# Kernel tuning notes

Measured on AMD Instinct MI355X. Metric: run time of the kernel, lower is better.

## Reference

```python
import jax, jax.numpy as jnp
import numpy as np

B, F, K, DEPTH = 512, 64, 64, 3  # feas == k == 64, deepDepth == 3


def setup_inputs() -> dict:
    key = jax.random.key(0)
    ks = jax.random.split(key, 16)
    x = jax.random.normal(ks[0], (B, F), dtype=jnp.float32)
    # wide: Linear(feas, 1)
    Ww = jax.random.normal(ks[1], (1, F), dtype=jnp.float32) * 0.1
    bw = jnp.zeros((1,), dtype=jnp.float32)
    # cross: Parameter(torch.rand(feas, k))
    cross = jax.random.uniform(ks[2], (F, K), dtype=jnp.float32)
    # attention: Linear(k, k) -> ReLU -> Linear(k, 1, bias=False)
    W1 = jax.random.normal(ks[3], (K, K), dtype=jnp.float32) / np.sqrt(K)
    b1 = jnp.zeros((K,), dtype=jnp.float32)
    w2 = jax.random.normal(ks[4], (K,), dtype=jnp.float32) / np.sqrt(K)
    # deep{i}: Linear(k//i, k//(i+1)) + ReLU, i = 1..DEPTH  -> 64->32->21->16
    dims = [K // i for i in range(1, DEPTH + 2)]  # [64, 32, 21, 16]
    Wd1 = jax.random.normal(ks[5], (dims[1], dims[0]), dtype=jnp.float32) / np.sqrt(dims[0])
    bd1 = jnp.zeros((dims[1],), dtype=jnp.float32)
    Wd2 = jax.random.normal(ks[6], (dims[2], dims[1]), dtype=jnp.float32) / np.sqrt(dims[1])
    bd2 = jnp.zeros((dims[2],), dtype=jnp.float32)
    Wd3 = jax.random.normal(ks[7], (dims[3], dims[2]), dtype=jnp.float32) / np.sqrt(dims[2])
    bd3 = jnp.zeros((dims[3],), dtype=jnp.float32)
    # out: Linear(feas // (deepDepth+1), 1) == Linear(16, 1)
    Wo = jax.random.normal(ks[8], (1, F // (DEPTH + 1)), dtype=jnp.float32) * 0.1
    bo = jnp.zeros((1,), dtype=jnp.float32)
    return {"x": x, "Ww": Ww, "bw": bw, "cross": cross, "W1": W1, "b1": b1,
            "w2": w2, "Wd1": Wd1, "bd1": bd1, "Wd2": Wd2, "bd2": bd2,
            "Wd3": Wd3, "bd3": bd3, "Wo": Wo, "bo": bo}


def reference(x, Ww, bw, cross, W1, b1, w2, Wd1, bd1, Wd2, bd2, Wd3, bd3, Wo, bo):
    linear = x @ Ww.T + bw  # [B, 1]

    # Pairwise FM interactions v[b,i,j,:] = x_i * x_j * (cross_i ∘ cross_j)
    xx = x[:, :, None] * x[:, None, :]                    # [B, F, F]
    cp = cross[:, None, :] * cross[None, :, :]            # [F, F, K]
    v = xx[..., None] * cp[None]                          # [B, F, F, K]

    # attention MLP score per pair
    h = jax.nn.relu(jnp.einsum('bijk,lk->bijl', v, W1) + b1)
    s = jnp.einsum('bijl,l->bij', h, w2)                  # [B, F, F]

    # loop semantics: upper triangle (j >= i), pair kept iff x_i != 0 and x_j != 0
    valid = jnp.triu(jnp.ones((F, F), dtype=bool))[None] \
        & (x[:, :, None] != 0) & (x[:, None, :] != 0)     # [B, F, F]
    neg = jnp.finfo(s.dtype).min
    logits = jnp.where(valid, s, neg)

    # softmax over [0 (seed zeros(1) entry), valid pair scores...];
    # the seed zeros(k) value-vector contributes nothing to the weighted sum.
    m = jnp.maximum(jnp.max(logits, axis=(1, 2)), 0.0)    # [B]
    e = jnp.where(valid, jnp.exp(logits - m[:, None, None]), 0.0)
    denom = jnp.exp(-m) + jnp.sum(e, axis=(1, 2))         # +exp(-m) is the 0-logit term
    tmp = jnp.einsum('bij,bijk->bk', e, v) / denom[:, None]  # [B, K]

    tmp = jax.nn.relu(tmp @ Wd1.T + bd1)
    tmp = jax.nn.relu(tmp @ Wd2.T + bd2)
    tmp = jax.nn.relu(tmp @ Wd3.T + bd3)
    deep_out = tmp @ Wo.T + bo                            # [B, 1]
    return jax.nn.sigmoid(linear + deep_out)
```

## Files before the change

kernel.cpp:

```cpp
#include <hip/hip_runtime.h>
#include <math.h>


#define BB 512
#define FF 64
#define STR 68
#define NPAIRS 2080
#define THREADS 512
#define NIT2 65
#define NEG_BIG -3.402823466e38f

typedef _Float16 half8 __attribute__((ext_vector_type(8)));
typedef _Float16 half4 __attribute__((ext_vector_type(4)));
typedef float f32x4 __attribute__((ext_vector_type(4)));

__device__ __forceinline__ half8 ld8(const _Float16* p) {
    half8 v;
    *(half4*)&v       = *(const half4*)p;
    *((half4*)&v + 1) = *(const half4*)(p + 4);
    return v;
}

__global__ __launch_bounds__(THREADS, 4) void afm_r5_kernel(
    const float* __restrict__ x,
    const float* __restrict__ Ww,
    const float* __restrict__ bw,
    const float* __restrict__ cross,
    const float* __restrict__ W1,
    const float* __restrict__ b1,
    const float* __restrict__ w2,
    const float* __restrict__ Wd1,
    const float* __restrict__ bd1,
    const float* __restrict__ Wd2,
    const float* __restrict__ bd2,
    const float* __restrict__ Wd3,
    const float* __restrict__ bd3,
    const float* __restrict__ Wo,
    const float* __restrict__ bo,
    float* __restrict__ out)
{
    __shared__ __align__(16) _Float16 ah_s [FF * STR];
    __shared__ __align__(16) _Float16 aht_s[FF * STR];
    __shared__ __align__(16) _Float16 M_s  [FF * STR];
    __shared__ float s_s[NPAIRS];
    __shared__ unsigned short lut_s[NPAIRS];
    __shared__ float x_sh[FF];
    __shared__ float part_s[4][FF];
    __shared__ float mlp_s[FF];
    __shared__ float red_s[16];

    const int tid  = threadIdx.x;
    const int lane = tid & 63;
    const int wave = tid >> 6;
    const int b    = blockIdx.x;
    const int m    = lane & 15;
    const int q    = lane >> 4;

    if (tid < FF) x_sh[tid] = x[b * FF + tid];
    __syncthreads();

    for (int idx = tid; idx < FF * FF; idx += THREADS) {
        const int i = idx >> 6, k = idx & 63;
        const _Float16 v = (_Float16)(x_sh[i] * cross[idx]);
        ah_s[i * STR + k]  = v;
        aht_s[k * STR + i] = v;
    }
    for (int idx = tid; idx < (FF * STR) / 2; idx += THREADS)
        ((int*)M_s)[idx] = 0;
    if (tid < FF) {
        const int i = tid;
        const int basei = i * FF - (i * (i - 1)) / 2;
        const bool xi = (x_sh[i] != 0.f);
        for (int j = i; j < FF; ++j) {
            const int valid = (xi && (x_sh[j] != 0.f)) ? 0x8000 : 0;
            lut_s[basei + (j - i)] = (unsigned short)((i << 8) | j | valid);
        }
    }

    half8 afr[4][2];
    #pragma unroll
    for (int mt = 0; mt < 4; ++mt)
        #pragma unroll
        for (int kt = 0; kt < 2; ++kt) {
            const float* wr = W1 + (mt * 16 + m) * FF + kt * 32 + q * 8;
            half8 h;
            #pragma unroll
            for (int jj = 0; jj < 8; ++jj) h[jj] = (_Float16)wr[jj];
            afr[mt][kt] = h;
        }
    float b1r[16], w2r[16];
    #pragma unroll
    for (int mt = 0; mt < 4; ++mt)
        #pragma unroll
        for (int r = 0; r < 4; ++r) {
            b1r[mt * 4 + r] = b1[mt * 16 + q * 4 + r];
            w2r[mt * 4 + r] = w2[mt * 16 + q * 4 + r];
        }
    __syncthreads();

    for (int it = wave; it < NIT2; it += 8) {
        const int p0 = it * 32;
        const int ijA = lut_s[p0 + m];
        const int ijB = lut_s[p0 + 16 + m];
        const int iA = (ijA >> 8) & 63, jA = ijA & 63;
        const int iB = (ijB >> 8) & 63, jB = ijB & 63;
        const half8 bA0 = ld8(&ah_s[iA * STR + q * 8])      * ld8(&ah_s[jA * STR + q * 8]);
        const half8 bA1 = ld8(&ah_s[iA * STR + 32 + q * 8]) * ld8(&ah_s[jA * STR + 32 + q * 8]);
        const half8 bB0 = ld8(&ah_s[iB * STR + q * 8])      * ld8(&ah_s[jB * STR + q * 8]);
        const half8 bB1 = ld8(&ah_s[iB * STR + 32 + q * 8]) * ld8(&ah_s[jB * STR + 32 + q * 8]);
        float spA = 0.f, spB = 0.f;
        #pragma unroll
        for (int mt = 0; mt < 4; ++mt) {
            f32x4 aA, aB;
            #pragma unroll
            for (int r = 0; r < 4; ++r) { aA[r] = b1r[mt * 4 + r]; aB[r] = b1r[mt * 4 + r]; }
            aA = __builtin_amdgcn_mfma_f32_16x16x32_f16(afr[mt][0], bA0, aA, 0, 0, 0);
            aB = __builtin_amdgcn_mfma_f32_16x16x32_f16(afr[mt][0], bB0, aB, 0, 0, 0);
            aA = __builtin_amdgcn_mfma_f32_16x16x32_f16(afr[mt][1], bA1, aA, 0, 0, 0);
            aB = __builtin_amdgcn_mfma_f32_16x16x32_f16(afr[mt][1], bB1, aB, 0, 0, 0);
            #pragma unroll
            for (int r = 0; r < 4; ++r) {
                spA = fmaf(w2r[mt * 4 + r], fmaxf(aA[r], 0.f), spA);
                spB = fmaf(w2r[mt * 4 + r], fmaxf(aB[r], 0.f), spB);
            }
        }
        spA += __shfl_xor(spA, 16, 64);
        spA += __shfl_xor(spA, 32, 64);
        spB += __shfl_xor(spB, 16, 64);
        spB += __shfl_xor(spB, 32, 64);
        if (lane < 16) {
            s_s[p0 + lane]      = (ijA & 0x8000) ? spA : NEG_BIG;
            s_s[p0 + 16 + lane] = (ijB & 0x8000) ? spB : NEG_BIG;
        }
    }
    __syncthreads();

    float mx = 0.0f;
    for (int p = tid; p < NPAIRS; p += THREADS) mx = fmaxf(mx, s_s[p]);
    #pragma unroll
    for (int off = 32; off > 0; off >>= 1)
        mx = fmaxf(mx, __shfl_xor(mx, off, 64));
    if (lane == 0) red_s[wave] = mx;
    __syncthreads();
    float mval = red_s[0];
    #pragma unroll
    for (int w = 1; w < 8; ++w) mval = fmaxf(mval, red_s[w]);

    float sum = 0.f;
    for (int p = tid; p < NPAIRS; p += THREADS) {
        const int ij = lut_s[p];
        const float e = __expf(s_s[p] - mval);
        sum += e;
        M_s[((ij >> 8) & 63) * STR + (ij & 63)] = (_Float16)e;
    }
    #pragma unroll
    for (int off = 32; off > 0; off >>= 1)
        sum += __shfl_xor(sum, off, 64);
    if (lane == 0) red_s[8 + wave] = sum;
    __syncthreads();
    float denom = __expf(-mval);
    #pragma unroll
    for (int w = 0; w < 8; ++w) denom += red_s[8 + w];

    {
        const int t0 = wave * 2;
        #pragma unroll
        for (int t = t0; t < t0 + 2; ++t) {
            const int i0 = (t >> 2) * 16, k0 = (t & 3) * 16;
            const half8 a0  = ld8(&M_s[(i0 + m) * STR + q * 8]);
            const half8 a1  = ld8(&M_s[(i0 + m) * STR + 32 + q * 8]);
            const half8 bb0 = ld8(&aht_s[(k0 + m) * STR + q * 8]);
            const half8 bb1 = ld8(&aht_s[(k0 + m) * STR + 32 + q * 8]);
            f32x4 g = {0.f, 0.f, 0.f, 0.f};
            g = __builtin_amdgcn_mfma_f32_16x16x32_f16(a0, bb0, g, 0, 0, 0);
            g = __builtin_amdgcn_mfma_f32_16x16x32_f16(a1, bb1, g, 0, 0, 0);
            const half4 ap = *(const half4*)&aht_s[(k0 + m) * STR + i0 + q * 4];
            float s4 = (float)ap[0] * g[0] + (float)ap[1] * g[1]
                     + (float)ap[2] * g[2] + (float)ap[3] * g[3];
            s4 += __shfl_xor(s4, 16, 64);
            s4 += __shfl_xor(s4, 32, 64);
            if (lane < 16) part_s[i0 >> 4][k0 + lane] = s4;
        }
    }
    __syncthreads();
    if (tid < FF)
        mlp_s[tid] = (part_s[0][tid] + part_s[1][tid] +
                      part_s[2][tid] + part_s[3][tid]) / denom;
    __syncthreads();

    float hv = 0.f;
    if (tid < 32) {
        float a1v = bd1[tid];
        for (int k = 0; k < 64; ++k) a1v = fmaf(Wd1[tid * 64 + k], mlp_s[k], a1v);
        hv = fmaxf(a1v, 0.f);
    }
    __syncthreads();
    if (tid < 32) mlp_s[tid] = hv;
    __syncthreads();
    if (tid < 21) {
        float a2 = bd2[tid];
        for (int k = 0; k < 32; ++k) a2 = fmaf(Wd2[tid * 32 + k], mlp_s[k], a2);
        hv = fmaxf(a2, 0.f);
    }
    __syncthreads();
    if (tid < 21) mlp_s[tid] = hv;
    __syncthreads();
    if (tid < 16) {
        float a3 = bd3[tid];
        for (int k = 0; k < 21; ++k) a3 = fmaf(Wd3[tid * 21 + k], mlp_s[k], a3);
        hv = fmaxf(a3, 0.f);
    }
    __syncthreads();
    if (tid < 16) mlp_s[tid] = hv;
    __syncthreads();

    if (tid == 0) {
        float deep = bo[0];
        for (int k = 0; k < 16; ++k) deep = fmaf(Wo[k], mlp_s[k], deep);
        float lin = bw[0];
        for (int k = 0; k < 64; ++k) lin = fmaf(Ww[k], x_sh[k], lin);
        const float z = lin + deep;
        out[b] = 1.f / (1.f + __expf(-z));
    }
}

extern "C" void kernel_launch(void* const* d_in, const int* in_sizes, int n_in,
                              void* d_out, int out_size, void* d_ws, size_t ws_size,
                              hipStream_t stream) {
    const float* xp    = (const float*)d_in[0];
    const float* Ww    = (const float*)d_in[1];
    const float* bw    = (const float*)d_in[2];
    const float* cross = (const float*)d_in[3];
    const float* W1    = (const float*)d_in[4];
    const float* b1    = (const float*)d_in[5];
    const float* w2    = (const float*)d_in[6];
    const float* Wd1   = (const float*)d_in[7];
    const float* bd1   = (const float*)d_in[8];
    const float* Wd2   = (const float*)d_in[9];
    const float* bd2   = (const float*)d_in[10];
    const float* Wd3   = (const float*)d_in[11];
    const float* bd3   = (const float*)d_in[12];
    const float* Wo    = (const float*)d_in[13];
    const float* bo    = (const float*)d_in[14];
    float* outp = (float*)d_out;

    afm_r5_kernel<<<BB, THREADS, 0, stream>>>(xp, Ww, bw, cross, W1, b1, w2,
                                              Wd1, bd1, Wd2, bd2, Wd3, bd3,
                                              Wo, bo, outp);
}
```

Before: 103.1 us.

## Parallelize LUT build, fuse softmax max into scoring, parallelize tail MLP

Builds the pair lookup table with all threads using a closed-form triangular index inversion instead of 64 serial threads. Folds the softmax max reduction into the scoring loop, which removes one shared-memory pass and one barrier, and applies the validity mask at the exp stage instead. Vectorizes the W1/b1/w2 parameter loads. Rewrites the deep MLP and output stages so several threads share each output and reduce with shuffles, replacing serial single-thread loops. The sqrt-based index inversion relies on float precision with a correction step.

```diff
diff --git a/kernel.cpp b/kernel.cpp
--- a/kernel.cpp
+++ b/kernel.cpp
@@ -21,7 +21,7 @@
     return v;
 }
 
-__global__ __launch_bounds__(THREADS, 4) void afm_r5_kernel(
+__global__ __launch_bounds__(THREADS, 4) void afm_r6_kernel(
     const float* __restrict__ x,
     const float* __restrict__ Ww,
     const float* __restrict__ bw,
@@ -67,14 +67,14 @@
     }
     for (int idx = tid; idx < (FF * STR) / 2; idx += THREADS)
         ((int*)M_s)[idx] = 0;
-    if (tid < FF) {
-        const int i = tid;
-        const int basei = i * FF - (i * (i - 1)) / 2;
-        const bool xi = (x_sh[i] != 0.f);
-        for (int j = i; j < FF; ++j) {
-            const int valid = (xi && (x_sh[j] != 0.f)) ? 0x8000 : 0;
-            lut_s[basei + (j - i)] = (unsigned short)((i << 8) | j | valid);
-        }
+    for (int p = tid; p < NPAIRS; p += THREADS) {
+        int i = (int)floorf((129.0f - sqrtf(16641.0f - 8.0f * (float)p)) * 0.5f);
+        int base = (i * (129 - i)) >> 1;
+        if (p < base) { --i; base = (i * (129 - i)) >> 1; }
+        else { const int nb = ((i + 1) * (128 - i)) >> 1; if (p >= nb) { ++i; base = nb; } }
+        const int j = i + (p - base);
+        const int valid = ((x_sh[i] != 0.f) && (x_sh[j] != 0.f)) ? 0x8000 : 0;
+        lut_s[p] = (unsigned short)((i << 8) | j | valid);
     }
 
     half8 afr[4][2];
@@ -83,21 +83,30 @@
         #pragma unroll
         for (int kt = 0; kt < 2; ++kt) {
             const float* wr = W1 + (mt * 16 + m) * FF + kt * 32 + q * 8;
+            const f32x4 w0 = *(const f32x4*)wr;
+            const f32x4 w1 = *(const f32x4*)(wr + 4);
             half8 h;
             #pragma unroll
-            for (int jj = 0; jj < 8; ++jj) h[jj] = (_Float16)wr[jj];
+            for (int jj = 0; jj < 4; ++jj) {
+                h[jj]     = (_Float16)w0[jj];
+                h[4 + jj] = (_Float16)w1[jj];
+            }
             afr[mt][kt] = h;
         }
     float b1r[16], w2r[16];
     #pragma unroll
-    for (int mt = 0; mt < 4; ++mt)
+    for (int mt = 0; mt < 4; ++mt) {
+        const f32x4 bb = *(const f32x4*)(b1 + mt * 16 + q * 4);
+        const f32x4 ww = *(const f32x4*)(w2 + mt * 16 + q * 4);
         #pragma unroll
         for (int r = 0; r < 4; ++r) {
-            b1r[mt * 4 + r] = b1[mt * 16 + q * 4 + r];
-            w2r[mt * 4 + r] = w2[mt * 16 + q * 4 + r];
-        }
-    __syncthreads();
-
+            b1r[mt * 4 + r] = bb[r];
+            w2r[mt * 4 + r] = ww[r];
+        }
+    }
+    __syncthreads();
+
+    float wave_mx = 0.0f;
     for (int it = wave; it < NIT2; it += 8) {
         const int p0 = it * 32;
         const int ijA = lut_s[p0 + m];
@@ -128,20 +137,20 @@
         spA += __shfl_xor(spA, 32, 64);
         spB += __shfl_xor(spB, 16, 64);
         spB += __shfl_xor(spB, 32, 64);
+        wave_mx = fmaxf(wave_mx, (ijA & 0x8000) ? spA : 0.f);
+        wave_mx = fmaxf(wave_mx, (ijB & 0x8000) ? spB : 0.f);
         if (lane < 16) {
-            s_s[p0 + lane]      = (ijA & 0x8000) ? spA : NEG_BIG;
-            s_s[p0 + 16 + lane] = (ijB & 0x8000) ? spB : NEG_BIG;
-        }
-    }
-    __syncthreads();
-
-    float mx = 0.0f;
-    for (int p = tid; p < NPAIRS; p += THREADS) mx = fmaxf(mx, s_s[p]);
-    #pragma unroll
-    for (int off = 32; off > 0; off >>= 1)
-        mx = fmaxf(mx, __shfl_xor(mx, off, 64));
-    if (lane == 0) red_s[wave] = mx;
-    __syncthreads();
+            s_s[p0 + lane]      = spA;
+            s_s[p0 + 16 + lane] = spB;
+        }
+    }
+    wave_mx = fmaxf(wave_mx, __shfl_xor(wave_mx, 1, 64));
+    wave_mx = fmaxf(wave_mx, __shfl_xor(wave_mx, 2, 64));
+    wave_mx = fmaxf(wave_mx, __shfl_xor(wave_mx, 4, 64));
+    wave_mx = fmaxf(wave_mx, __shfl_xor(wave_mx, 8, 64));
+    if (lane == 0) red_s[wave] = wave_mx;
+    __syncthreads();
+
     float mval = red_s[0];
     #pragma unroll
     for (int w = 1; w < 8; ++w) mval = fmaxf(mval, red_s[w]);
@@ -149,7 +158,7 @@
     float sum = 0.f;
     for (int p = tid; p < NPAIRS; p += THREADS) {
         const int ij = lut_s[p];
-        const float e = __expf(s_s[p] - mval);
+        const float e = (ij & 0x8000) ? __expf(s_s[p] - mval) : 0.f;
         sum += e;
         M_s[((ij >> 8) & 63) * STR + (ij & 63)] = (_Float16)e;
     }
@@ -188,39 +197,57 @@
                       part_s[2][tid] + part_s[3][tid]) / denom;
     __syncthreads();
 
-    float hv = 0.f;
-    if (tid < 32) {
-        float a1v = bd1[tid];
-        for (int k = 0; k < 64; ++k) a1v = fmaf(Wd1[tid * 64 + k], mlp_s[k], a1v);
-        hv = fmaxf(a1v, 0.f);
-    }
-    __syncthreads();
-    if (tid < 32) mlp_s[tid] = hv;
-    __syncthreads();
-    if (tid < 21) {
-        float a2 = bd2[tid];
-        for (int k = 0; k < 32; ++k) a2 = fmaf(Wd2[tid * 32 + k], mlp_s[k], a2);
-        hv = fmaxf(a2, 0.f);
-    }
-    __syncthreads();
-    if (tid < 21) mlp_s[tid] = hv;
-    __syncthreads();
-    if (tid < 16) {
-        float a3 = bd3[tid];
-        for (int k = 0; k < 21; ++k) a3 = fmaf(Wd3[tid * 21 + k], mlp_s[k], a3);
-        hv = fmaxf(a3, 0.f);
-    }
-    __syncthreads();
-    if (tid < 16) mlp_s[tid] = hv;
-    __syncthreads();
-
-    if (tid == 0) {
-        float deep = bo[0];
-        for (int k = 0; k < 16; ++k) deep = fmaf(Wo[k], mlp_s[k], deep);
-        float lin = bw[0];
-        for (int k = 0; k < 64; ++k) lin = fmaf(Ww[k], x_sh[k], lin);
-        const float z = lin + deep;
-        out[b] = 1.f / (1.f + __expf(-z));
+    float* tmp2 = part_s[0];
+
+    {
+        const int outi = tid >> 4, kp = tid & 15;
+        float a = 0.f;
+        #pragma unroll
+        for (int t = 0; t < 4; ++t)
+            a = fmaf(Wd1[outi * 64 + kp + t * 16], mlp_s[kp + t * 16], a);
+        a += __shfl_xor(a, 1, 64);
+        a += __shfl_xor(a, 2, 64);
+        a += __shfl_xor(a, 4, 64);
+        a += __shfl_xor(a, 8, 64);
+        if (kp == 0) tmp2[outi] = fmaxf(a + bd1[outi], 0.f);
+    }
+    __syncthreads();
+
+    if (tid < 21 * 8) {
+        const int outi = tid >> 3, kp = tid & 7;
+        float a = 0.f;
+        #pragma unroll
+        for (int t = 0; t < 4; ++t)
+            a = fmaf(Wd2[outi * 32 + kp + t * 8], tmp2[kp + t * 8], a);
+        a += __shfl_xor(a, 1, 64);
+        a += __shfl_xor(a, 2, 64);
+        a += __shfl_xor(a, 4, 64);
+        if (kp == 0) mlp_s[outi] = fmaxf(a + bd2[outi], 0.f);
+    }
+    __syncthreads();
+
+    if (tid < 16 * 8) {
+        const int outi = tid >> 3, kp = tid & 7;
+        float a = Wd3[outi * 21 + kp] * mlp_s[kp];
+        a = fmaf(Wd3[outi * 21 + kp + 8], mlp_s[kp + 8], a);
+        if (kp < 5) a = fmaf(Wd3[outi * 21 + kp + 16], mlp_s[kp + 16], a);
+        a += __shfl_xor(a, 1, 64);
+        a += __shfl_xor(a, 2, 64);
+        a += __shfl_xor(a, 4, 64);
+        if (kp == 0) tmp2[outi] = fmaxf(a + bd3[outi], 0.f);
+    }
+    __syncthreads();
+
+    if (wave == 0) {
+        float v = Ww[lane] * x_sh[lane];
+        if (lane < 16) v = fmaf(Wo[lane], tmp2[lane], v);
+        #pragma unroll
+        for (int off = 32; off > 0; off >>= 1)
+            v += __shfl_xor(v, off, 64);
+        if (lane == 0) {
+            const float z = v + bw[0] + bo[0];
+            out[b] = 1.f / (1.f + __expf(-z));
+        }
     }
 }
 
@@ -244,7 +271,7 @@
     const float* bo    = (const float*)d_in[14];
     float* outp = (float*)d_out;
 
-    afm_r5_kernel<<<BB, THREADS, 0, stream>>>(xp, Ww, bw, cross, W1, b1, w2,
+    afm_r6_kernel<<<BB, THREADS, 0, stream>>>(xp, Ww, bw, cross, W1, b1, w2,
                                               Wd1, bd1, Wd2, bd2, Wd3, bd3,
                                               Wo, bo, outp);
 }
```

Measured after the change: 103.3 us. No clear change (+0.2%).
